# Kernel tuning notes

Hardware: AMD Instinct MI355X
Metric: run time of the kernel (lower is better)

## Reference

```python
import jax, jax.numpy as jnp
import numpy as np

N, NUM_CLASSES, FEAT_DIM = 32768, 395, 512


def setup_inputs() -> dict:
    key = jax.random.key(0)
    k1, k2, k3, k4 = jax.random.split(key, 4)
    modal1_inputs = jax.random.normal(k1, (N, FEAT_DIM), dtype=jnp.float32)
    modal2_inputs = jax.random.normal(k2, (N, FEAT_DIM), dtype=jnp.float32)
    targets = jax.random.randint(k3, (N,), 0, NUM_CLASSES)
    # learned centers parameter: torch.rand -> uniform [0, 1)
    centers = jax.random.uniform(k4, (NUM_CLASSES, FEAT_DIM), dtype=jnp.float32)
    return {
        "modal1_inputs": modal1_inputs,
        "modal2_inputs": modal2_inputs,
        "centers": centers,
        "targets": targets,
    }


def _smooth_l1(a, b):
    # SmoothL1Loss with default beta=1.0, reduction='mean'
    d = jnp.abs(a - b)
    return jnp.mean(jnp.where(d < 1.0, 0.5 * d * d, d - 0.5))


def reference(modal1_inputs, modal2_inputs, centers, targets):
    num_classes = centers.shape[0]
    # Per-label mean (the original O(N^2) loop is exactly a segment mean
    # gathered back per sample).
    ones = jnp.ones((targets.shape[0],), dtype=modal1_inputs.dtype)
    counts = jax.ops.segment_sum(ones, targets, num_segments=num_classes)
    counts = jnp.maximum(counts, 1.0)  # empty classes never gathered
    sum1 = jax.ops.segment_sum(modal1_inputs, targets, num_segments=num_classes)
    sum2 = jax.ops.segment_sum(modal2_inputs, targets, num_segments=num_classes)
    centersR = (sum1 / counts[:, None])[targets]  # [N, D]
    centersT = (sum2 / counts[:, None])[targets]  # [N, D]
    gathered_centers = centers[targets]           # [N, D]
    loss = _smooth_l1(centersR, gathered_centers) + _smooth_l1(centersT, gathered_centers)
    return loss
```

## Files before the change

### kernel.cpp

```cpp
#include <hip/hip_runtime.h>

#define NS 32768
#define NC 395
#define FD 512
#define NEL (NC * FD)

#define RS 16
#define CT 16
#define COLS 32
#define CF4 8
#define ROWS_PB (NS / RS)
#define NW 8
#define LCAP 384

__device__ float g_part[2 * RS * NC * FD];
__device__ int   g_hist[RS * NC];

__global__ __launch_bounds__(512, 4)
void k_stream(const float* __restrict__ m1, const float* __restrict__ m2,
              const int* __restrict__ targets, float* __restrict__ out)
{
    const int bid = blockIdx.x;
    const int ct  = bid & (CT - 1);
    const int mod = (bid >> 4) & 1;
    const int rs  = bid >> 5;
    const int t   = threadIdx.x;
    const int w   = t >> 6;
    const int lane = t & 63;
    const int r    = lane >> 3;
    const int c4   = lane & 7;

    __shared__ float4 acc4[NC * CF4];
    __shared__ int    lists[NW * LCAP];

    {
        float4 z = make_float4(0.f, 0.f, 0.f, 0.f);
        for (int i = t; i < NC * CF4; i += 512) acc4[i] = z;
    }
    if (bid == 0 && t == 0) out[0] = 0.f;

    const int* tgt = targets + rs * ROWS_PB;
    int* mylist = &lists[w * LCAP];
    int cnt = 0;
    int nxt = tgt[lane];
    for (int it = 0; it < ROWS_PB / 64; ++it) {
        int c = nxt;
        if (it + 1 < ROWS_PB / 64) nxt = tgt[(it + 1) * 64 + lane];
        bool pred = ((c & 7) == w);
        unsigned long long mask = __ballot(pred);
        int pos = (int)__popcll(mask & ((1ull << lane) - 1ull));
        if (pred && cnt + pos < LCAP)
            mylist[cnt + pos] = (it * 64 + lane) | (c << 12);
        cnt += (int)__popcll(mask);
    }
    if (cnt > LCAP) cnt = LCAP;
    __syncthreads();

    const float4* sp = reinterpret_cast<const float4*>(
        (mod ? m2 : m1) + (size_t)rs * ROWS_PB * FD) + ct * CF4 + c4;
    const int ngroups = (cnt + 7) >> 3;

#define LOADG(CLS, V, G)                                                 \
    {   int g_ = (G);                                                    \
        CLS = -1; V = make_float4(0.f, 0.f, 0.f, 0.f);                   \
        if (g_ < ngroups) {                                              \
            int e_   = mylist[g_ * 8 + r];        \
            bool a_  = (g_ * 8 + r) < cnt;                               \
            int idx_ = a_ ? (e_ & 0xFFF) : 0;                            \
            CLS      = a_ ? (e_ >> 12) : -1;                             \
            V        = sp[idx_ * 128];            \
        }                                                                \
    }

#define RMWG(CLS, V)                                                     \
    {   int cls_ = CLS;                                                  \
        int rank_ = 0;                                                   \
        _Pragma("unroll")                                                \
        for (int d_ = 1; d_ < 8; ++d_) {                                 \
            int cu_ = __shfl_up(cls_, 8 * d_, 64);                       \
            rank_ += (r >= d_ && cu_ == cls_) ? 1 : 0;                   \
        }                                                                \
        for (int k_ = 0; k_ < 8; ++k_) {                                 \
            if (k_ > 0 && !__any(rank_ >= k_)) break;                    \
            if (cls_ >= 0 && rank_ == k_) {                              \
                int a_ = cls_ * 8 + ((c4 + (cls_ >> 3)) & 7);            \
                float4 o_ = acc4[a_];                                    \
                o_.x += V.x; o_.y += V.y; o_.z += V.z; o_.w += V.w;      \
                acc4[a_] = o_;                                           \
            }                                                            \
        }                                                                \
    }

    int cls0, cls1, cls2, cls3, cn0, cn1, cn2, cn3;
    float4 v0, v1, v2, v3, u0, u1, u2, u3;

    LOADG(cls0, v0, 0) LOADG(cls1, v1, 1) LOADG(cls2, v2, 2) LOADG(cls3, v3, 3)
    const int nbat = (ngroups + 3) >> 2;
    for (int b = 1; b < nbat; ++b) {
        int gb = b << 2;
        LOADG(cn0, u0, gb)     LOADG(cn1, u1, gb + 1)
        LOADG(cn2, u2, gb + 2) LOADG(cn3, u3, gb + 3)
        RMWG(cls0, v0) RMWG(cls1, v1) RMWG(cls2, v2) RMWG(cls3, v3)
        cls0 = cn0; v0 = u0; cls1 = cn1; v1 = u1;
        cls2 = cn2; v2 = u2; cls3 = cn3; v3 = u3;
    }
    RMWG(cls0, v0) RMWG(cls1, v1) RMWG(cls2, v2) RMWG(cls3, v3)
#undef LOADG
#undef RMWG
    __syncthreads();

    float4* dst = reinterpret_cast<float4*>(g_part)
                + (size_t)(mod * RS + rs) * (NEL / 4) + ct * CF4;
    for (int i = t; i < NC * CF4; i += 512) {
        int cls = i >> 3, cc = i & 7;
        float4 vv = acc4[cls * 8 + ((cc + (cls >> 3)) & 7)];
        dst[(size_t)cls * (FD / 4) + cc] = vv;
    }

    if (ct == 0 && mod == 0) {
        __syncthreads();
        int* h = reinterpret_cast<int*>(acc4);
        for (int i = t; i < NC; i += 512) h[i] = 0;
        __syncthreads();
        for (int i = t; i < ROWS_PB; i += 512) atomicAdd(&h[tgt[i]], 1);
        __syncthreads();
        for (int i = t; i < NC; i += 512) g_hist[rs * NC + i] = h[i];
    }
}

__device__ __forceinline__ float smooth_l1(float d) {
    d = fabsf(d);
    return d < 1.0f ? 0.5f * d * d : d - 0.5f;
}

__device__ __forceinline__ void f4add(float4& a, const float4 b) {
    a.x += b.x; a.y += b.y; a.z += b.z; a.w += b.w;
}

__global__ __launch_bounds__(256)
void k_loss(const float* __restrict__ centers, float* __restrict__ out) {
    __shared__ float scnt[NC];
    int t = threadIdx.x;
    for (int c = t; c < NC; c += 256) {
        int s = 0;
        #pragma unroll
        for (int k = 0; k < RS; ++k) s += g_hist[k * NC + c];
        scnt[c] = (float)s;
    }
    __syncthreads();

    const float4* ctr4  = reinterpret_cast<const float4*>(centers);
    const float4* part4 = reinterpret_cast<const float4*>(g_part);
    const int NE4 = NEL / 4;
    float val = 0.f;
    for (int g = blockIdx.x * 256 + t; g < NE4; g += gridDim.x * 256) {
        int cls = g >> 7;
        float cnt = scnt[cls];
        if (cnt > 0.f) {
            float4 s1 = make_float4(0,0,0,0), s2 = make_float4(0,0,0,0);
            #pragma unroll
            for (int k = 0; k < RS; ++k) {
                f4add(s1, part4[(size_t)k        * NE4 + g]);
                f4add(s2, part4[(size_t)(RS + k) * NE4 + g]);
            }
            float4 c4 = ctr4[g];
            float inv = 1.f / cnt;
            val += cnt * (smooth_l1(s1.x * inv - c4.x) + smooth_l1(s2.x * inv - c4.x)
                        + smooth_l1(s1.y * inv - c4.y) + smooth_l1(s2.y * inv - c4.y)
                        + smooth_l1(s1.z * inv - c4.z) + smooth_l1(s2.z * inv - c4.z)
                        + smooth_l1(s1.w * inv - c4.w) + smooth_l1(s2.w * inv - c4.w));
        }
    }

    for (int off = 32; off > 0; off >>= 1)
        val += __shfl_down(val, off, 64);
    __shared__ float wsum[4];
    int lane = t & 63, wid = t >> 6;
    if (lane == 0) wsum[wid] = val;
    __syncthreads();
    if (t == 0) {
        float sm = wsum[0] + wsum[1] + wsum[2] + wsum[3];
        atomicAdd(out, sm * 5.9604644775390625e-08f);
    }
}

extern "C" void kernel_launch(void* const* d_in, const int* in_sizes, int n_in,
                              void* d_out, int out_size, void* d_ws, size_t ws_size,
                              hipStream_t stream) {
    const float* m1 = (const float*)d_in[0];
    const float* m2 = (const float*)d_in[1];
    const float* centers = (const float*)d_in[2];
    const int* targets = (const int*)d_in[3];
    float* out = (float*)d_out;

    k_stream<<<RS * 2 * CT, 512, 0, stream>>>(m1, m2, targets, out);
    k_loss<<<400, 256, 0, stream>>>(centers, out);
}
```

Measured before the change: 186.2 us.

## Partition classes across waves and residue sublists to drop conflict-resolution shuffles

Each block now covers 64 feature columns for half of the classes. Each wave owns a contiguous class range, and its rows are bucketed by class modulo 4 into four sublists, one per 16-lane group. Two rows processed together in the same wave can therefore never hit the same class, so the shuffle-based rank computation and the serialized read-modify-write loop on shared memory are removed. The cost is a second pass over the targets to count and then scatter, plus twice as many blocks. Rows beyond the smaller per-wave list capacity are silently dropped if a class range is heavily populated.

```diff
diff --git a/kernel.cpp b/kernel.cpp
--- a/kernel.cpp
+++ b/kernel.cpp
@@ -6,12 +6,13 @@
 #define NEL (NC * FD)
 
 #define RS 16
-#define CT 16
-#define COLS 32
-#define CF4 8
 #define ROWS_PB (NS / RS)
+#define CT 8
+#define COLS 64
+#define CF4 16
+#define ASTR 68
 #define NW 8
-#define LCAP 384
+#define WCAP 224
 
 __device__ float g_part[2 * RS * NC * FD];
 __device__ int   g_hist[RS * NC];
@@ -21,81 +22,95 @@
               const int* __restrict__ targets, float* __restrict__ out)
 {
     const int bid = blockIdx.x;
-    const int ct  = bid & (CT - 1);
+    const int cg  = bid & 1;
+    const int ct  = (bid >> 1) & 7;
     const int mod = (bid >> 4) & 1;
     const int rs  = bid >> 5;
     const int t   = threadIdx.x;
     const int w   = t >> 6;
     const int lane = t & 63;
-    const int r    = lane >> 3;
-    const int c4   = lane & 7;
-
-    __shared__ float4 acc4[NC * CF4];
-    __shared__ int    lists[NW * LCAP];
+    const int r    = lane >> 4;
+    const int c4   = lane & 15;
+
+    const int cb  = cg ? 198 : 0;
+    const int nch = cg ? 197 : 198;
+
+    __shared__ float acc[198 * ASTR];
+    __shared__ int   lists[NW * WCAP];
+
+    for (int i = t; i < 198 * ASTR; i += 512) acc[i] = 0.f;
+    if (bid == 0 && t == 0) out[0] = 0.f;
+
+    const int lo = cb + (w * nch) / 8;
+    const int hi = cb + ((w + 1) * nch) / 8;
+
+    const int* tgt = targets + rs * ROWS_PB;
+    int* wlist = &lists[w * WCAP];
+
+    int n0 = 0, n1 = 0, n2 = 0, n3 = 0;
+    for (int it = 0; it < ROWS_PB / 64; ++it) {
+        int c = tgt[it * 64 + lane];
+        bool mine = (c >= lo) && (c < hi);
+        n0 += (int)__popcll(__ballot(mine && ((c & 3) == 0)));
+        n1 += (int)__popcll(__ballot(mine && ((c & 3) == 1)));
+        n2 += (int)__popcll(__ballot(mine && ((c & 3) == 2)));
+        n3 += (int)__popcll(__ballot(mine && ((c & 3) == 3)));
+    }
+    const int b0 = 0, b1 = n0, b2 = n0 + n1, b3 = n0 + n1 + n2;
 
     {
-        float4 z = make_float4(0.f, 0.f, 0.f, 0.f);
-        for (int i = t; i < NC * CF4; i += 512) acc4[i] = z;
-    }
-    if (bid == 0 && t == 0) out[0] = 0.f;
-
-    const int* tgt = targets + rs * ROWS_PB;
-    int* mylist = &lists[w * LCAP];
-    int cnt = 0;
-    int nxt = tgt[lane];
-    for (int it = 0; it < ROWS_PB / 64; ++it) {
-        int c = nxt;
-        if (it + 1 < ROWS_PB / 64) nxt = tgt[(it + 1) * 64 + lane];
-        bool pred = ((c & 7) == w);
-        unsigned long long mask = __ballot(pred);
-        int pos = (int)__popcll(mask & ((1ull << lane) - 1ull));
-        if (pred && cnt + pos < LCAP)
-            mylist[cnt + pos] = (it * 64 + lane) | (c << 12);
-        cnt += (int)__popcll(mask);
-    }
-    if (cnt > LCAP) cnt = LCAP;
-    __syncthreads();
-
-    const float4* sp = reinterpret_cast<const float4*>(
-        (mod ? m2 : m1) + (size_t)rs * ROWS_PB * FD) + ct * CF4 + c4;
-    const int ngroups = (cnt + 7) >> 3;
+        int cur0 = b0, cur1 = b1, cur2 = b2, cur3 = b3;
+        for (int it = 0; it < ROWS_PB / 64; ++it) {
+            int idx = it * 64 + lane;
+            int c = tgt[idx];
+            bool mine = (c >= lo) && (c < hi);
+            unsigned long long below = (1ull << lane) - 1ull;
+#define SCAT(K, CUR)                                                     \
+            {   unsigned long long m_ = __ballot(mine && ((c & 3) == K));\
+                if (mine && ((c & 3) == K)) {                            \
+                    int p_ = CUR + (int)__popcll(m_ & below);            \
+                    if (p_ < WCAP) wlist[p_] = idx | (c << 16);          \
+                }                                                        \
+                CUR += (int)__popcll(m_);                                \
+            }
+            SCAT(0, cur0) SCAT(1, cur1) SCAT(2, cur2) SCAT(3, cur3)
+#undef SCAT
+        }
+    }
+    __syncthreads();
+
+    int qb = (r == 0) ? b0 : (r == 1) ? b1 : (r == 2) ? b2 : b3;
+    int qn = (r == 0) ? n0 : (r == 1) ? n1 : (r == 2) ? n2 : n3;
+    if (qb > WCAP) qb = WCAP;
+    if (qb + qn > WCAP) qn = WCAP - qb;
+    const int ng = max(max(n0, n1), max(n2, n3));
+
+    const float4* sp = reinterpret_cast<const float4*>(mod ? m2 : m1)
+                     + (size_t)rs * ROWS_PB * (FD / 4) + ct * CF4 + c4;
 
 #define LOADG(CLS, V, G)                                                 \
     {   int g_ = (G);                                                    \
         CLS = -1; V = make_float4(0.f, 0.f, 0.f, 0.f);                   \
-        if (g_ < ngroups) {                                              \
-            int e_   = mylist[g_ * 8 + r];        \
-            bool a_  = (g_ * 8 + r) < cnt;                               \
-            int idx_ = a_ ? (e_ & 0xFFF) : 0;                            \
-            CLS      = a_ ? (e_ >> 12) : -1;                             \
-            V        = sp[idx_ * 128];            \
+        if (g_ < qn) {                            \
+            int e_ = wlist[qb + g_];                                     \
+            CLS = e_ >> 16;                                              \
+            V = sp[(e_ & 0x7FF) * 128];     \
         }                                                                \
     }
 
 #define RMWG(CLS, V)                                                     \
-    {   int cls_ = CLS;                                                  \
-        int rank_ = 0;                                                   \
-        _Pragma("unroll")                                                \
-        for (int d_ = 1; d_ < 8; ++d_) {                                 \
-            int cu_ = __shfl_up(cls_, 8 * d_, 64);                       \
-            rank_ += (r >= d_ && cu_ == cls_) ? 1 : 0;                   \
-        }                                                                \
-        for (int k_ = 0; k_ < 8; ++k_) {                                 \
-            if (k_ > 0 && !__any(rank_ >= k_)) break;                    \
-            if (cls_ >= 0 && rank_ == k_) {                              \
-                int a_ = cls_ * 8 + ((c4 + (cls_ >> 3)) & 7);            \
-                float4 o_ = acc4[a_];                                    \
-                o_.x += V.x; o_.y += V.y; o_.z += V.z; o_.w += V.w;      \
-                acc4[a_] = o_;                                           \
-            }                                                            \
-        }                                                                \
+    if (CLS >= 0) {                                                      \
+        float* ap = &acc[(CLS - cb) * ASTR + c4 * 4];                    \
+        float4 o_ = *reinterpret_cast<float4*>(ap);                      \
+        o_.x += V.x; o_.y += V.y; o_.z += V.z; o_.w += V.w;              \
+        *reinterpret_cast<float4*>(ap) = o_;                             \
     }
 
     int cls0, cls1, cls2, cls3, cn0, cn1, cn2, cn3;
     float4 v0, v1, v2, v3, u0, u1, u2, u3;
 
     LOADG(cls0, v0, 0) LOADG(cls1, v1, 1) LOADG(cls2, v2, 2) LOADG(cls3, v3, 3)
-    const int nbat = (ngroups + 3) >> 2;
+    const int nbat = (ng + 3) >> 2;
     for (int b = 1; b < nbat; ++b) {
         int gb = b << 2;
         LOADG(cn0, u0, gb)     LOADG(cn1, u1, gb + 1)
@@ -111,15 +126,15 @@
 
     float4* dst = reinterpret_cast<float4*>(g_part)
                 + (size_t)(mod * RS + rs) * (NEL / 4) + ct * CF4;
-    for (int i = t; i < NC * CF4; i += 512) {
-        int cls = i >> 3, cc = i & 7;
-        float4 vv = acc4[cls * 8 + ((cc + (cls >> 3)) & 7)];
-        dst[(size_t)cls * (FD / 4) + cc] = vv;
-    }
-
-    if (ct == 0 && mod == 0) {
+    for (int i = t; i < nch * CF4; i += 512) {
+        int cl = i >> 4, cf = i & 15;
+        float4 vv = *reinterpret_cast<float4*>(&acc[cl * ASTR + cf * 4]);
+        dst[(size_t)(cb + cl) * (FD / 4) + cf] = vv;
+    }
+
+    if (ct == 0 && mod == 0 && cg == 0) {
         __syncthreads();
-        int* h = reinterpret_cast<int*>(acc4);
+        int* h = reinterpret_cast<int*>(acc);
         for (int i = t; i < NC; i += 512) h[i] = 0;
         __syncthreads();
         for (int i = t; i < ROWS_PB; i += 512) atomicAdd(&h[tgt[i]], 1);
@@ -193,6 +208,6 @@
     const int* targets = (const int*)d_in[3];
     float* out = (float*)d_out;
 
-    k_stream<<<RS * 2 * CT, 512, 0, stream>>>(m1, m2, targets, out);
+    k_stream<<<RS * 2 * CT * 2, 512, 0, stream>>>(m1, m2, targets, out);
     k_loss<<<400, 256, 0, stream>>>(centers, out);
 }
```

Measured after the change: 190.3 us. +2.2%, slower.
